# Kernel optimization log

Measured on AMD Instinct MI355X. Metric: run time of the kernel, lower is better.

## Reference

```python
import jax, jax.numpy as jnp
import numpy as np

NPOINT = 1024
RADIUS = 0.2
NSAMPLE = 32
BN_EPS = 1e-5


def setup_inputs() -> dict:
    key = jax.random.key(0)
    ks = jax.random.split(key, 8)
    B, N, D = 16, 8192, 9
    xyz = jax.random.uniform(ks[0], (B, N, 3), dtype=jnp.float32)
    points = jax.random.normal(ks[1], (B, N, D), dtype=jnp.float32)
    chans = [D, 64, 64, 128]
    inp = {"xyz": xyz, "points": points}
    for i in range(3):
        cin, cout = chans[i], chans[i + 1]
        inp[f"W{i}"] = jax.random.normal(ks[2 + i], (cout, cin), dtype=jnp.float32) / np.sqrt(cin).astype(np.float32)
        inp[f"b{i}"] = jnp.zeros((cout,), jnp.float32)
        inp[f"gamma{i}"] = jnp.ones((cout,), jnp.float32)
        inp[f"beta{i}"] = jnp.zeros((cout,), jnp.float32)
    return inp


def farthest_point_sample(xyz, npoint):
    # xyz: [B,N,3]. Sequential FPS via lax.scan (deterministic start at index 0).
    B, N, _ = xyz.shape
    dist0 = jnp.full((B, N), 1e10, xyz.dtype)
    far0 = jnp.zeros((B,), jnp.int32)

    def step(carry, _):
        distance, farthest = carry
        centroid = jnp.take_along_axis(xyz, farthest[:, None, None], axis=1)  # [B,1,3]
        d = jnp.sum((xyz - centroid) ** 2, axis=-1)  # [B,N]
        distance = jnp.minimum(distance, d)
        return (distance, jnp.argmax(distance, axis=-1).astype(jnp.int32)), farthest

    (_, _), cents = jax.lax.scan(step, (dist0, far0), None, length=npoint)
    return cents.T  # [B,npoint]


def gather_points(points, idx):
    # points [B,N,C], idx [B,...] -> [B,...,C]
    return jax.vmap(lambda p, i: p[i])(points, idx)


def query_ball_point(radius, nsample, xyz, new_xyz):
    # pairwise squared distances [B,S,N]
    sqr = (jnp.sum(new_xyz ** 2, -1)[:, :, None]
           + jnp.sum(xyz ** 2, -1)[:, None, :]
           - 2.0 * jnp.einsum('bsc,bnc->bsn', new_xyz, xyz))
    negd, idx = jax.lax.top_k(-sqr, nsample)  # nsample nearest, ascending distance
    d = -negd
    first = idx[:, :, :1]
    return jnp.where(d > radius ** 2, first, idx)  # [B,S,nsample]


def reference(xyz, points, W0, b0, gamma0, beta0, W1, b1, gamma1, beta1, W2, b2, gamma2, beta2):
    cent = farthest_point_sample(xyz, NPOINT)          # [B,S]
    new_xyz = gather_points(xyz, cent)                  # [B,S,3]
    idx = query_ball_point(RADIUS, NSAMPLE, xyz, new_xyz)
    x = gather_points(points, idx)                      # [B,S,K,D]
    x = jnp.transpose(x, (0, 3, 2, 1))                  # [B,D,K,S]
    for W, b, g, be in ((W0, b0, gamma0, beta0), (W1, b1, gamma1, beta1), (W2, b2, gamma2, beta2)):
        x = jnp.einsum('oc,bcks->boks', W, x) + b[None, :, None, None]
        mean = x.mean(axis=(0, 2, 3), keepdims=True)    # training-mode BatchNorm2d
        var = x.var(axis=(0, 2, 3), keepdims=True)
        x = (x - mean) * jax.lax.rsqrt(var + BN_EPS) * g[None, :, None, None] + be[None, :, None, None]
        x = jax.nn.relu(x)
    feat = jnp.max(x, axis=2)                           # max over nsample -> [B,C,S]
    return new_xyz, jnp.transpose(feat, (0, 2, 1))      # [B,S,3], [B,S,128]
```

## Files before the change

### kernel.cpp

```cpp
#include <hip/hip_runtime.h>
#include <cstddef>
#include <cstdint>


#define BB 16
#define NN 8192
#define DD 9
#define SS 1024
#define KK 32
#define M_COLS (BB*SS*KK)
#define C1 64
#define C2 64
#define C3 128
#define NBKT 64
#define NG 54

#define WSB_IDX   0
#define WSB_STATS (WSB_IDX + M_COLS*2)
#define WSB_AFF   (WSB_STATS + 32768*4)
#define WSB_WT    (WSB_AFF + 512*4)
#define WSB_END   (WSB_WT + 12864*4)
#define PG1 0
#define PS2 (2*NBKT*C1)
#define PQ2 (3*NBKT*C1)
#define PS3 (4*NBKT*C1)
#define PQ3 (PS3 + NBKT*C3)

#define FPS_T   512
#define FPS_PPT (NN/FPS_T)
#define FPS_W   (FPS_T/64)

__global__ __launch_bounds__(FPS_T) void fps_kernel(const float* __restrict__ xyz,
                                                    float* __restrict__ out_newxyz) {
    __shared__ float sx[NN], sy[NN], sz[NN];
    __shared__ int   sfar[SS];
    __shared__ unsigned long long rp[2][FPS_W];
    const int b = blockIdx.x, tid = threadIdx.x;
    const int wave = tid >> 6, lane = tid & 63;
    const float* base = xyz + (size_t)b * NN * 3;
    for (int i = tid; i < NN; i += FPS_T) {
        sx[i] = base[i*3+0];
        sy[i] = base[i*3+1];
        sz[i] = base[i*3+2];
    }
    __syncthreads();
    float px[FPS_PPT], py[FPS_PPT], pz[FPS_PPT], dist[FPS_PPT];
#pragma unroll
    for (int m = 0; m < FPS_PPT; ++m) {
        int i = tid + m*FPS_T;
        px[m] = sx[i]; py[m] = sy[i]; pz[m] = sz[i];
        dist[m] = 1e10f;
    }
    if (tid == 0) sfar[0] = 0;
    float cx = sx[0], cy = sy[0], cz = sz[0];
    for (int it = 1; it < SS; ++it) {
        float lv = -1.0f; int lm = 0;
#pragma unroll
        for (int m = 0; m < FPS_PPT; ++m) {
            float dx = px[m]-cx, dy = py[m]-cy, dz = pz[m]-cz;
            float d  = fmaf(dz, dz, fmaf(dy, dy, dx*dx));
            float nd = fminf(dist[m], d);
            dist[m] = nd;
            if (nd > lv) { lv = nd; lm = m; }
        }
        int li = tid + lm*FPS_T;
        unsigned long long pk = ((unsigned long long)__float_as_uint(lv) << 32)
                              | (unsigned int)(NN - 1 - li);
#pragma unroll
        for (int msk = 1; msk < 64; msk <<= 1) {
            unsigned long long o = __shfl_xor(pk, msk, 64);
            pk = (o > pk) ? o : pk;
        }
        const int pb = it & 1;
        if (lane == 0) rp[pb][wave] = pk;
        __syncthreads();
        unsigned long long bp = rp[pb][0];
#pragma unroll
        for (int w = 1; w < FPS_W; ++w) {
            unsigned long long o = rp[pb][w];
            bp = (o > bp) ? o : bp;
        }
        int bi = NN - 1 - (int)(unsigned int)(bp & 0xFFFFFFFFull);
        if (tid == 0) sfar[it] = bi;
        cx = sx[bi]; cy = sy[bi]; cz = sz[bi];
    }
    __syncthreads();
    for (int s = tid; s < SS; s += FPS_T) {
        int nidx = sfar[s];
        out_newxyz[((size_t)b*SS + s)*3 + 0] = sx[nidx];
        out_newxyz[((size_t)b*SS + s)*3 + 1] = sy[nidx];
        out_newxyz[((size_t)b*SS + s)*3 + 2] = sz[nidx];
    }
}

__device__ __forceinline__ unsigned fmap(float f) {
    unsigned u = __float_as_uint(f);
    return u ^ (unsigned)(((int)u >> 31) | 0x80000000);
}
#define PK_INF 0xFFFFFFFFFFFFFFFFull

__global__ __launch_bounds__(64) void query_kernel(const float* __restrict__ xyz,
                                                   const float* __restrict__ newxyz,
                                                   unsigned short* __restrict__ idx_out) {
    __shared__ unsigned bm[NN/32];
    const int blk  = blockIdx.x;
    const int b    = blk >> 10;
    const int lane = threadIdx.x;
    for (int i = lane; i < NN/32; i += 64) bm[i] = 0;
    const float cx = newxyz[(size_t)blk*3+0];
    const float cy = newxyz[(size_t)blk*3+1];
    const float cz = newxyz[(size_t)blk*3+2];
    const float s2 = fmaf(cz, cz, fmaf(cy, cy, cx*cx));
    const float* xb = xyz + (size_t)b*NN*3;
    float lv = 3.0e38f; int li = 0;
    for (int m = 0; m < NN/64; ++m) {
        int j = lane + m*64;
        float x = xb[(size_t)j*3+0], y = xb[(size_t)j*3+1], z = xb[(size_t)j*3+2];
        float n2  = fmaf(z, z, fmaf(y, y, x*x));
        float dot = fmaf(cz, z, fmaf(cy, y, cx*x));
        float sq  = (s2 + n2) - 2.0f*dot;
        if (sq < lv) { lv = sq; li = j; }
    }
    __syncthreads();
    unsigned long long lpk = ((unsigned long long)fmap(lv) << 32) | (unsigned)li;
    unsigned long long g = lpk;
#pragma unroll
    for (int msk = 1; msk < 64; msk <<= 1) {
        unsigned long long o = __shfl_xor(g, msk, 64);
        g = (o < g) ? o : g;
    }
    const unsigned R2M = fmap(0.04f);
    int first_idx = 0, out_idx = 0;
    for (int k = 0; k < KK; ++k) {
        int wi = (int)(unsigned)(g & 0xFFFFFFFFull);
        unsigned wm = (unsigned)(g >> 32);
        if (k == 0) first_idx = wi;
        int keep = (wm > R2M) ? first_idx : wi;
        if (lane == k) out_idx = keep;
        int owner = wi & 63;
        if (lane == owner) bm[wi >> 5] |= (1u << (wi & 31));
        __syncthreads();
        int j0 = owner + ((2*lane) << 6);
        int j1 = j0 + 64;
        float x0 = xb[(size_t)j0*3+0], y0 = xb[(size_t)j0*3+1], z0 = xb[(size_t)j0*3+2];
        float x1 = xb[(size_t)j1*3+0], y1 = xb[(size_t)j1*3+1], z1 = xb[(size_t)j1*3+2];
        float sq0 = (s2 + fmaf(z0, z0, fmaf(y0, y0, x0*x0))) - 2.0f*fmaf(cz, z0, fmaf(cy, y0, cx*x0));
        float sq1 = (s2 + fmaf(z1, z1, fmaf(y1, y1, x1*x1))) - 2.0f*fmaf(cz, z1, fmaf(cy, y1, cx*x1));
        bool t0 = (bm[j0 >> 5] >> (j0 & 31)) & 1;
        bool t1 = (bm[j1 >> 5] >> (j1 & 31)) & 1;
        unsigned long long p0 = t0 ? PK_INF : (((unsigned long long)fmap(sq0) << 32) | (unsigned)j0);
        unsigned long long p1 = t1 ? PK_INF : (((unsigned long long)fmap(sq1) << 32) | (unsigned)j1);
        unsigned long long r = (p1 < p0) ? p1 : p0;
        unsigned long long c = (lane == owner) ? PK_INF : lpk;
        c = (r < c) ? r : c;
#pragma unroll
        for (int msk = 1; msk < 64; msk <<= 1) {
            unsigned long long ro = __shfl_xor(r, msk, 64);
            unsigned long long co = __shfl_xor(c, msk, 64);
            r = (ro < r) ? ro : r;
            c = (co < c) ? co : c;
        }
        if (lane == owner) lpk = r;
        g = c;
        __syncthreads();
    }
    if (lane < KK) idx_out[(size_t)blk*KK + lane] = (unsigned short)out_idx;
}

__global__ void transpose_w_kernel(const float* __restrict__ W0, const float* __restrict__ W1,
                                   const float* __restrict__ W2, float* __restrict__ w0t,
                                   float* __restrict__ w1t, float* __restrict__ w2t) {
    int t = blockIdx.x*256 + threadIdx.x;
    if (t < DD*C1)  { int c = t / C1, o = t % C1; w0t[t] = W0[o*DD + c]; }
    if (t < C1*C2)  { int c = t / C2, o = t % C2; w1t[t] = W1[o*C1 + c]; }
    if (t < C1*C3)  { int c = t / C3, o = t % C3; w2t[t] = W2[o*C1 + c]; }
}

__global__ __launch_bounds__(256) void gram_kernel(const float* __restrict__ points,
                                                   const unsigned short* __restrict__ idxw,
                                                   float* __restrict__ pg) {
    __shared__ float sg[NG];
    const int tid = threadIdx.x, lane = tid & 63;
    float acc[NG];
#pragma unroll
    for (int t = 0; t < NG; ++t) acc[t] = 0.f;
#pragma unroll
    for (int i = 0; i < 4; ++i) {
        int col = blockIdx.x*1024 + i*256 + tid;
        int n = idxw[col];
        int b = col >> 15;
        const float* p = points + ((size_t)b*NN + n)*DD;
        float x[DD];
#pragma unroll
        for (int c = 0; c < DD; ++c) x[c] = p[c];
#pragma unroll
        for (int c = 0; c < DD; ++c) acc[c] += x[c];
        int t = DD;
#pragma unroll
        for (int c = 0; c < DD; ++c)
#pragma unroll
            for (int d = c; d < DD; ++d) { acc[t] = fmaf(x[c], x[d], acc[t]); ++t; }
    }
#pragma unroll
    for (int t = 0; t < NG; ++t) {
#pragma unroll
        for (int msk = 1; msk < 64; msk <<= 1) acc[t] += __shfl_xor(acc[t], msk, 64);
    }
    if (tid < NG) sg[tid] = 0.f;
    __syncthreads();
    if (lane == 0) {
#pragma unroll
        for (int t = 0; t < NG; ++t) atomicAdd(&sg[t], acc[t]);
    }
    __syncthreads();
    int bkt = blockIdx.x & (NBKT-1);
    if (tid < NG) atomicAdd(&pg[bkt*64 + tid], sg[tid]);
}

__global__ void affine1_kernel(const float* __restrict__ pg,
                               const float* __restrict__ W0, const float* __restrict__ b0,
                               const float* __restrict__ gamma, const float* __restrict__ beta,
                               float* __restrict__ scale, float* __restrict__ shift) {
    __shared__ float sm[NG];
    int tid = threadIdx.x;
    if (tid < NG) {
        float s = 0.f;
        for (int b = 0; b < NBKT; ++b) s += pg[b*64 + tid];
        sm[tid] = s;
    }
    __syncthreads();
    if (tid < C1) {
        float w[DD];
#pragma unroll
        for (int i = 0; i < DD; ++i) w[i] = W0[tid*DD + i];
        float mv = 0.f;
#pragma unroll
        for (int i = 0; i < DD; ++i) mv = fmaf(w[i], sm[i], mv);
        float q = 0.f;
        int t = DD;
#pragma unroll
        for (int c = 0; c < DD; ++c)
#pragma unroll
            for (int d = c; d < DD; ++d) {
                float coef = w[c]*w[d];
                if (c != d) coef = coef + coef;
                q = fmaf(coef, sm[t], q); ++t;
            }
        float b0v = b0[tid];
        const float M = (float)M_COLS;
        float s_sum = mv + M*b0v;
        float s_sq  = q + 2.f*b0v*mv + M*b0v*b0v;
        const float invM = 1.0f / M;
        float mean = s_sum * invM;
        float var  = s_sq * invM - mean*mean;
        float sc   = gamma[tid] / sqrtf(var + 1e-5f);
        scale[tid] = sc;
        shift[tid] = beta[tid] - mean*sc;
    }
}

__device__ __forceinline__ void stats_accumulate64(const float* acc,
                                                   float* __restrict__ g_sum,
                                                   float* __restrict__ g_sq) {
    __shared__ float s_sum[C1];
    __shared__ float s_sq[C1];
    int tid = threadIdx.x, lane = tid & 63;
    if (tid < C1) { s_sum[tid] = 0.f; s_sq[tid] = 0.f; }
    __syncthreads();
#pragma unroll
    for (int o = 0; o < C1; ++o) {
        float v = acc[o];
        float q = v*v;
#pragma unroll
        for (int msk = 1; msk < 64; msk <<= 1) {
            v += __shfl_xor(v, msk, 64);
            q += __shfl_xor(q, msk, 64);
        }
        if (lane == 0) { atomicAdd(&s_sum[o], v); atomicAdd(&s_sq[o], q); }
    }
    __syncthreads();
    if (tid < C1) { atomicAdd(&g_sum[tid], s_sum[tid]); atomicAdd(&g_sq[tid], s_sq[tid]); }
    __syncthreads();
}

__device__ __forceinline__ void gather_conv1(const float* __restrict__ points,
                                             const unsigned short* __restrict__ idxw,
                                             const float* __restrict__ w0t,
                                             const float* __restrict__ b0,
                                             int col, float (&a1)[C1]) {
    int n = idxw[col];
    int b = col >> 15;
    const float* p = points + ((size_t)b*NN + n)*DD;
    float x[DD];
#pragma unroll
    for (int c = 0; c < DD; ++c) x[c] = p[c];
#pragma unroll
    for (int o = 0; o < C1; ++o) a1[o] = b0[o];
#pragma unroll
    for (int c = 0; c < DD; ++c) {
        float xc = x[c];
#pragma unroll
        for (int o = 0; o < C1; ++o) a1[o] = fmaf(w0t[c*C1+o], xc, a1[o]);
    }
}

__device__ __forceinline__ void conv2_from_a1(float (&a1)[C1],
                                              const float* __restrict__ sc1,
                                              const float* __restrict__ sh1,
                                              const float* __restrict__ w1t,
                                              const float* __restrict__ b1,
                                              float (&a2)[C2]) {
#pragma unroll
    for (int c = 0; c < C1; ++c) a1[c] = fmaxf(fmaf(a1[c], sc1[c], sh1[c]), 0.0f);
#pragma unroll
    for (int o = 0; o < C2; ++o) a2[o] = b1[o];
    for (int c = 0; c < C1; ++c) {
        float xc = a1[c];
#pragma unroll
        for (int o = 0; o < C2; ++o) a2[o] = fmaf(w1t[c*C2+o], xc, a2[o]);
    }
}

__global__ void affine_kernel(const float* __restrict__ psum, const float* __restrict__ psq,
                              const float* __restrict__ gamma, const float* __restrict__ beta,
                              float* __restrict__ scale, float* __restrict__ shift, int nch) {
    int i = threadIdx.x;
    if (i < nch) {
        float s = 0.f, q = 0.f;
        for (int b = 0; b < NBKT; ++b) { s += psum[b*nch + i]; q += psq[b*nch + i]; }
        const float invM = 1.0f / (float)M_COLS;
        float mean = s * invM;
        float var  = q * invM - mean*mean;
        float sc   = gamma[i] / sqrtf(var + 1e-5f);
        scale[i] = sc;
        shift[i] = beta[i] - mean*sc;
    }
}

__global__ __launch_bounds__(256) void pass2_kernel(const float* __restrict__ points,
                                                    const unsigned short* __restrict__ idxw,
                                                    const float* __restrict__ w0t,
                                                    const float* __restrict__ b0,
                                                    const float* __restrict__ sc1,
                                                    const float* __restrict__ sh1,
                                                    const float* __restrict__ w1t,
                                                    const float* __restrict__ b1,
                                                    float* __restrict__ pstats) {
    int col = blockIdx.x*256 + threadIdx.x;
    int bkt = blockIdx.x & (NBKT-1);
    float a1[C1], a2[C2];
    gather_conv1(points, idxw, w0t, b0, col, a1);
    conv2_from_a1(a1, sc1, sh1, w1t, b1, a2);
    stats_accumulate64(a2, pstats + PS2 + bkt*C1, pstats + PQ2 + bkt*C1);
}

__global__ __launch_bounds__(256) void pass34_kernel(const float* __restrict__ points,
                                                     const unsigned short* __restrict__ idxw,
                                                     const float* __restrict__ w0t,
                                                     const float* __restrict__ b0,
                                                     const float* __restrict__ sc1,
                                                     const float* __restrict__ sh1,
                                                     const float* __restrict__ w1t,
                                                     const float* __restrict__ b1,
                                                     const float* __restrict__ sc2,
                                                     const float* __restrict__ sh2,
                                                     const float* __restrict__ w2t,
                                                     const float* __restrict__ b2,
                                                     const float* __restrict__ gamma2,
                                                     float* __restrict__ pool_out,
                                                     float* __restrict__ pstats) {
    int col = blockIdx.x*256 + threadIdx.x;
    int bkt = blockIdx.x & (NBKT-1);
    float a1[C1], a2[C2];
    gather_conv1(points, idxw, w0t, b0, col, a1);
    conv2_from_a1(a1, sc1, sh1, w1t, b1, a2);
#pragma unroll
    for (int c = 0; c < C2; ++c) a2[c] = fmaxf(fmaf(a2[c], sc2[c], sh2[c]), 0.0f);
    int lane = threadIdx.x & 63;
    int bs = col >> 5;
#pragma unroll
    for (int h = 0; h < 2; ++h) {
        float acc[C1];
#pragma unroll
        for (int o = 0; o < C1; ++o) acc[o] = b2[h*C1+o];
        for (int c = 0; c < C2; ++c) {
            float xc = a2[c];
#pragma unroll
            for (int o = 0; o < C1; ++o) acc[o] = fmaf(w2t[c*C3 + h*C1 + o], xc, acc[o]);
        }
#pragma unroll
        for (int o = 0; o < C1; ++o) {
            bool pos = gamma2[h*C1+o] >= 0.f;
            float v = pos ? acc[o] : -acc[o];
#pragma unroll
            for (int msk = 1; msk < 32; msk <<= 1) v = fmaxf(v, __shfl_xor(v, msk, 64));
            if ((lane & 31) == 0) pool_out[(size_t)bs*C3 + h*C1 + o] = pos ? v : -v;
        }
        stats_accumulate64(acc, pstats + PS3 + bkt*C3 + h*C1, pstats + PQ3 + bkt*C3 + h*C1);
    }
}

__global__ __launch_bounds__(256) void bn3relu_kernel(float* __restrict__ pool,
                                                      const float* __restrict__ sc3,
                                                      const float* __restrict__ sh3) {
    int e = blockIdx.x*256 + threadIdx.x;
    int ch = e & (C3-1);
    float v = pool[e];
    pool[e] = fmaxf(fmaf(v, sc3[ch], sh3[ch]), 0.0f);
}

extern "C" void kernel_launch(void* const* d_in, const int* in_sizes, int n_in,
                              void* d_out, int out_size, void* d_ws, size_t ws_size,
                              hipStream_t stream) {
    const float* xyz    = (const float*)d_in[0];
    const float* points = (const float*)d_in[1];
    const float* W0     = (const float*)d_in[2];
    const float* b0     = (const float*)d_in[3];
    const float* gamma0 = (const float*)d_in[4];
    const float* beta0  = (const float*)d_in[5];
    const float* W1     = (const float*)d_in[6];
    const float* b1     = (const float*)d_in[7];
    const float* gamma1 = (const float*)d_in[8];
    const float* beta1  = (const float*)d_in[9];
    const float* W2     = (const float*)d_in[10];
    const float* b2     = (const float*)d_in[11];
    const float* gamma2 = (const float*)d_in[12];
    const float* beta2  = (const float*)d_in[13];

    char* wsb = (char*)d_ws;
    unsigned short* idxw = (unsigned short*)(wsb + WSB_IDX);
    float* pstats = (float*)(wsb + WSB_STATS);
    float* aff = (float*)(wsb + WSB_AFF);
    float* sc1 = aff,       *sh1 = aff + 64;
    float* sc2 = aff + 128, *sh2 = aff + 192;
    float* sc3 = aff + 256, *sh3 = aff + 384;
    float* wT  = (float*)(wsb + WSB_WT);
    float* w0t = wT, *w1t = wT + DD*C1, *w2t = wT + DD*C1 + C1*C2;

    float* out_newxyz = (float*)d_out;
    float* out_feat   = (float*)d_out + (size_t)BB*SS*3;

    hipMemsetAsync(pstats, 0, 32768*sizeof(float), stream);
    fps_kernel<<<dim3(BB), dim3(FPS_T), 0, stream>>>(xyz, out_newxyz);
    transpose_w_kernel<<<dim3(32), dim3(256), 0, stream>>>(W0, W1, W2, w0t, w1t, w2t);
    query_kernel<<<dim3(BB*SS), dim3(64), 0, stream>>>(xyz, out_newxyz, idxw);
    gram_kernel<<<dim3(M_COLS/1024), dim3(256), 0, stream>>>(points, idxw, pstats + PG1);
    affine1_kernel<<<dim3(1), dim3(64), 0, stream>>>(pstats + PG1, W0, b0, gamma0, beta0, sc1, sh1);
    pass2_kernel<<<dim3(M_COLS/256), dim3(256), 0, stream>>>(points, idxw, w0t, b0, sc1, sh1, w1t, b1, pstats);
    affine_kernel<<<dim3(1), dim3(128), 0, stream>>>(pstats + PS2, pstats + PQ2, gamma1, beta1, sc2, sh2, C2);
    pass34_kernel<<<dim3(M_COLS/256), dim3(256), 0, stream>>>(points, idxw, w0t, b0, sc1, sh1, w1t, b1, sc2, sh2, w2t, b2, gamma2, out_feat, pstats);
    affine_kernel<<<dim3(1), dim3(128), 0, stream>>>(pstats + PS3, pstats + PQ3, gamma2, beta2, sc3, sh3, C3);
    bn3relu_kernel<<<dim3((BB*SS*C3)/256), dim3(256), 0, stream>>>(out_feat, sc3, sh3);
}
```

Before: 1.889 ms.

## Cache conv2 activations in workspace and use float ballot argmax in FPS

Pass2 can now store the pre-BN conv2 output to a large workspace buffer. Pass34 then reads it back instead of redoing the point gather and the first two convolutions. This path is only taken when the workspace is large enough, and it trades recomputation for about 256MB of extra memory traffic. The FPS wave argmax now does a 32-bit float max reduction plus a ballot-based index tie-break instead of a 64-bit packed shuffle reduction.

```diff
diff --git a/kernel.cpp b/kernel.cpp
--- a/kernel.cpp
+++ b/kernel.cpp
@@ -20,6 +20,7 @@
 #define WSB_AFF   (WSB_STATS + 32768*4)
 #define WSB_WT    (WSB_AFF + 512*4)
 #define WSB_END   (WSB_WT + 12864*4)
+#define WSB_Y2    ((WSB_END + 255) & ~255)
 #define PG1 0
 #define PS2 (2*NBKT*C1)
 #define PQ2 (3*NBKT*C1)
@@ -64,13 +65,25 @@
             if (nd > lv) { lv = nd; lm = m; }
         }
         int li = tid + lm*FPS_T;
-        unsigned long long pk = ((unsigned long long)__float_as_uint(lv) << 32)
-                              | (unsigned int)(NN - 1 - li);
-#pragma unroll
-        for (int msk = 1; msk < 64; msk <<= 1) {
-            unsigned long long o = __shfl_xor(pk, msk, 64);
-            pk = (o > pk) ? o : pk;
-        }
+        float wv = lv;
+#pragma unroll
+        for (int msk = 1; msk < 64; msk <<= 1) wv = fmaxf(wv, __shfl_xor(wv, msk, 64));
+        unsigned long long tied = __ballot(lv == wv);
+        int wli;
+        if ((tied & (tied - 1)) == 0) {
+            int src = __ffsll((unsigned long long)tied) - 1;
+            wli = __shfl(li, src, 64);
+        } else {
+            int cand = (lv == wv) ? li : 0x7FFFFFFF;
+#pragma unroll
+            for (int msk = 1; msk < 64; msk <<= 1) {
+                int o = __shfl_xor(cand, msk, 64);
+                cand = (o < cand) ? o : cand;
+            }
+            wli = cand;
+        }
+        unsigned long long pk = ((unsigned long long)__float_as_uint(wv) << 32)
+                              | (unsigned int)(NN - 1 - wli);
         const int pb = it & 1;
         if (lane == 0) rp[pb][wave] = pk;
         __syncthreads();
@@ -337,6 +350,29 @@
     }
 }
 
+template<bool STORE>
+__device__ __forceinline__ void pass2_body(const float* __restrict__ points,
+                                           const unsigned short* __restrict__ idxw,
+                                           const float* __restrict__ w0t,
+                                           const float* __restrict__ b0,
+                                           const float* __restrict__ sc1,
+                                           const float* __restrict__ sh1,
+                                           const float* __restrict__ w1t,
+                                           const float* __restrict__ b1,
+                                           float* __restrict__ Y2,
+                                           float* __restrict__ pstats) {
+    int col = blockIdx.x*256 + threadIdx.x;
+    int bkt = blockIdx.x & (NBKT-1);
+    float a1[C1], a2[C2];
+    gather_conv1(points, idxw, w0t, b0, col, a1);
+    conv2_from_a1(a1, sc1, sh1, w1t, b1, a2);
+    if (STORE) {
+#pragma unroll
+        for (int o = 0; o < C2; ++o) Y2[(size_t)o*M_COLS + col] = a2[o];
+    }
+    stats_accumulate64(a2, pstats + PS2 + bkt*C1, pstats + PQ2 + bkt*C1);
+}
+
 __global__ __launch_bounds__(256) void pass2_kernel(const float* __restrict__ points,
                                                     const unsigned short* __restrict__ idxw,
                                                     const float* __restrict__ w0t,
@@ -346,12 +382,56 @@
                                                     const float* __restrict__ w1t,
                                                     const float* __restrict__ b1,
                                                     float* __restrict__ pstats) {
+    pass2_body<false>(points, idxw, w0t, b0, sc1, sh1, w1t, b1, nullptr, pstats);
+}
+
+__global__ __launch_bounds__(256) void pass2_store_kernel(const float* __restrict__ points,
+                                                          const unsigned short* __restrict__ idxw,
+                                                          const float* __restrict__ w0t,
+                                                          const float* __restrict__ b0,
+                                                          const float* __restrict__ sc1,
+                                                          const float* __restrict__ sh1,
+                                                          const float* __restrict__ w1t,
+                                                          const float* __restrict__ b1,
+                                                          float* __restrict__ Y2,
+                                                          float* __restrict__ pstats) {
+    pass2_body<true>(points, idxw, w0t, b0, sc1, sh1, w1t, b1, Y2, pstats);
+}
+
+__device__ __forceinline__ void pass34_tail(float (&a2)[C2],
+                                            const float* __restrict__ sc2,
+                                            const float* __restrict__ sh2,
+                                            const float* __restrict__ w2t,
+                                            const float* __restrict__ b2,
+                                            const float* __restrict__ gamma2,
+                                            float* __restrict__ pool_out,
+                                            float* __restrict__ pstats) {
+#pragma unroll
+    for (int c = 0; c < C2; ++c) a2[c] = fmaxf(fmaf(a2[c], sc2[c], sh2[c]), 0.0f);
     int col = blockIdx.x*256 + threadIdx.x;
     int bkt = blockIdx.x & (NBKT-1);
-    float a1[C1], a2[C2];
-    gather_conv1(points, idxw, w0t, b0, col, a1);
-    conv2_from_a1(a1, sc1, sh1, w1t, b1, a2);
-    stats_accumulate64(a2, pstats + PS2 + bkt*C1, pstats + PQ2 + bkt*C1);
+    int lane = threadIdx.x & 63;
+    int bs = col >> 5;
+#pragma unroll
+    for (int h = 0; h < 2; ++h) {
+        float acc[C1];
+#pragma unroll
+        for (int o = 0; o < C1; ++o) acc[o] = b2[h*C1+o];
+        for (int c = 0; c < C2; ++c) {
+            float xc = a2[c];
+#pragma unroll
+            for (int o = 0; o < C1; ++o) acc[o] = fmaf(w2t[c*C3 + h*C1 + o], xc, acc[o]);
+        }
+#pragma unroll
+        for (int o = 0; o < C1; ++o) {
+            bool pos = gamma2[h*C1+o] >= 0.f;
+            float v = pos ? acc[o] : -acc[o];
+#pragma unroll
+            for (int msk = 1; msk < 32; msk <<= 1) v = fmaxf(v, __shfl_xor(v, msk, 64));
+            if ((lane & 31) == 0) pool_out[(size_t)bs*C3 + h*C1 + o] = pos ? v : -v;
+        }
+        stats_accumulate64(acc, pstats + PS3 + bkt*C3 + h*C1, pstats + PQ3 + bkt*C3 + h*C1);
+    }
 }
 
 __global__ __launch_bounds__(256) void pass34_kernel(const float* __restrict__ points,
@@ -370,34 +450,25 @@
                                                      float* __restrict__ pool_out,
                                                      float* __restrict__ pstats) {
     int col = blockIdx.x*256 + threadIdx.x;
-    int bkt = blockIdx.x & (NBKT-1);
     float a1[C1], a2[C2];
     gather_conv1(points, idxw, w0t, b0, col, a1);
     conv2_from_a1(a1, sc1, sh1, w1t, b1, a2);
-#pragma unroll
-    for (int c = 0; c < C2; ++c) a2[c] = fmaxf(fmaf(a2[c], sc2[c], sh2[c]), 0.0f);
-    int lane = threadIdx.x & 63;
-    int bs = col >> 5;
-#pragma unroll
-    for (int h = 0; h < 2; ++h) {
-        float acc[C1];
-#pragma unroll
-        for (int o = 0; o < C1; ++o) acc[o] = b2[h*C1+o];
-        for (int c = 0; c < C2; ++c) {
-            float xc = a2[c];
-#pragma unroll
-            for (int o = 0; o < C1; ++o) acc[o] = fmaf(w2t[c*C3 + h*C1 + o], xc, acc[o]);
-        }
-#pragma unroll
-        for (int o = 0; o < C1; ++o) {
-            bool pos = gamma2[h*C1+o] >= 0.f;
-            float v = pos ? acc[o] : -acc[o];
-#pragma unroll
-            for (int msk = 1; msk < 32; msk <<= 1) v = fmaxf(v, __shfl_xor(v, msk, 64));
-            if ((lane & 31) == 0) pool_out[(size_t)bs*C3 + h*C1 + o] = pos ? v : -v;
-        }
-        stats_accumulate64(acc, pstats + PS3 + bkt*C3 + h*C1, pstats + PQ3 + bkt*C3 + h*C1);
-    }
+    pass34_tail(a2, sc2, sh2, w2t, b2, gamma2, pool_out, pstats);
+}
+
+__global__ __launch_bounds__(256) void pass34_cached_kernel(const float* __restrict__ Y2,
+                                                            const float* __restrict__ sc2,
+                                                            const float* __restrict__ sh2,
+                                                            const float* __restrict__ w2t,
+                                                            const float* __restrict__ b2,
+                                                            const float* __restrict__ gamma2,
+                                                            float* __restrict__ pool_out,
+                                                            float* __restrict__ pstats) {
+    int col = blockIdx.x*256 + threadIdx.x;
+    float a2[C2];
+#pragma unroll
+    for (int o = 0; o < C2; ++o) a2[o] = Y2[(size_t)o*M_COLS + col];
+    pass34_tail(a2, sc2, sh2, w2t, b2, gamma2, pool_out, pstats);
 }
 
 __global__ __launch_bounds__(256) void bn3relu_kernel(float* __restrict__ pool,
@@ -436,6 +507,8 @@
     float* sc3 = aff + 256, *sh3 = aff + 384;
     float* wT  = (float*)(wsb + WSB_WT);
     float* w0t = wT, *w1t = wT + DD*C1, *w2t = wT + DD*C1 + C1*C2;
+    float* Y2  = (float*)(wsb + WSB_Y2);
+    const bool use_y2 = ws_size >= (size_t)WSB_Y2 + (size_t)C2 * M_COLS * 4;
 
     float* out_newxyz = (float*)d_out;
     float* out_feat   = (float*)d_out + (size_t)BB*SS*3;
@@ -446,9 +519,15 @@
     query_kernel<<<dim3(BB*SS), dim3(64), 0, stream>>>(xyz, out_newxyz, idxw);
     gram_kernel<<<dim3(M_COLS/1024), dim3(256), 0, stream>>>(points, idxw, pstats + PG1);
     affine1_kernel<<<dim3(1), dim3(64), 0, stream>>>(pstats + PG1, W0, b0, gamma0, beta0, sc1, sh1);
-    pass2_kernel<<<dim3(M_COLS/256), dim3(256), 0, stream>>>(points, idxw, w0t, b0, sc1, sh1, w1t, b1, pstats);
-    affine_kernel<<<dim3(1), dim3(128), 0, stream>>>(pstats + PS2, pstats + PQ2, gamma1, beta1, sc2, sh2, C2);
-    pass34_kernel<<<dim3(M_COLS/256), dim3(256), 0, stream>>>(points, idxw, w0t, b0, sc1, sh1, w1t, b1, sc2, sh2, w2t, b2, gamma2, out_feat, pstats);
+    if (use_y2) {
+        pass2_store_kernel<<<dim3(M_COLS/256), dim3(256), 0, stream>>>(points, idxw, w0t, b0, sc1, sh1, w1t, b1, Y2, pstats);
+        affine_kernel<<<dim3(1), dim3(128), 0, stream>>>(pstats + PS2, pstats + PQ2, gamma1, beta1, sc2, sh2, C2);
+        pass34_cached_kernel<<<dim3(M_COLS/256), dim3(256), 0, stream>>>(Y2, sc2, sh2, w2t, b2, gamma2, out_feat, pstats);
+    } else {
+        pass2_kernel<<<dim3(M_COLS/256), dim3(256), 0, stream>>>(points, idxw, w0t, b0, sc1, sh1, w1t, b1, pstats);
+        affine_kernel<<<dim3(1), dim3(128), 0, stream>>>(pstats + PS2, pstats + PQ2, gamma1, beta1, sc2, sh2, C2);
+        pass34_kernel<<<dim3(M_COLS/256), dim3(256), 0, stream>>>(points, idxw, w0t, b0, sc1, sh1, w1t, b1, sc2, sh2, w2t, b2, gamma2, out_feat, pstats);
+    }
     affine_kernel<<<dim3(1), dim3(128), 0, stream>>>(pstats + PS3, pstats + PQ3, gamma2, beta2, sc3, sh3, C3);
     bn3relu_kernel<<<dim3((BB*SS*C3)/256), dim3(256), 0, stream>>>(out_feat, sc3, sh3);
 }
```

Measured after the change: 2.000 ms. +5.9%, slower.
